# Kernel optimization log

Hardware: AMD Instinct MI355X
Metric: run time of the kernel (lower is better)

## Reference

```python
import jax, jax.numpy as jnp
import numpy as np

N_PROTS = 20000
N_GRAPHS = 16
N = N_PROTS * N_GRAPHS        # 320_000 nodes
F = 128                       # input features
L = 10                        # lat_size (hard-coded in module)
E = 10_240_000                # edges, avg degree 32


def setup_inputs() -> dict:
    key = jax.random.key(0)
    ks = jax.random.split(key, 8)
    x = jax.random.normal(ks[0], (N, F), dtype=jnp.float32)
    edge_index = jax.random.randint(ks[1], (2, E), 0, N, dtype=jnp.int32)
    def lin(k, fan_in, shape):
        return jax.random.uniform(k, shape, jnp.float32, -1.0, 1.0) / np.sqrt(fan_in)
    return {
        "x": x,
        "edge_index": edge_index,
        "W_in": lin(ks[2], F, (F, L)),
        "b_in": jnp.zeros((L,), jnp.float32),
        "W1": lin(ks[3], L, (L, L)),
        "b1": jnp.zeros((L,), jnp.float32),
        "W2": lin(ks[4], L, (L, L)),
        "b2": jnp.zeros((L,), jnp.float32),
        "W_out": lin(ks[5], L, (L, 1)),
        "b_out": jnp.zeros((1,), jnp.float32),
    }


def _gcn_improved(h, row, col, deg_inv_sqrt, W, b):
    # GCNConv(improved=True): A_hat = A + 2I, out = D^-1/2 A_hat D^-1/2 (h W) + b
    hw = h @ W                                   # [N, L]
    norm = deg_inv_sqrt[row] * deg_inv_sqrt[col]  # [E]
    agg = jax.ops.segment_sum(norm[:, None] * hw[row], col, num_segments=N)
    # self-loop with weight 2: contributes 2/deg * hw per node
    agg = agg + (2.0 * deg_inv_sqrt * deg_inv_sqrt)[:, None] * hw
    return agg + b


def reference(x, edge_index, W_in, b_in, W1, b1, W2, b2, W_out, b_out):
    row, col = edge_index[0], edge_index[1]
    # degree incl. self-loop fill value 2.0 (improved)
    deg = jax.ops.segment_sum(jnp.ones((E,), jnp.float32), col, num_segments=N) + 2.0
    deg_inv_sqrt = jax.lax.rsqrt(deg)

    h = jax.nn.relu(x @ W_in + b_in)                         # input_linear + relu
    h = jax.nn.relu(_gcn_improved(h, row, col, deg_inv_sqrt, W1, b1))
    h = jax.nn.relu(_gcn_improved(h, row, col, deg_inv_sqrt, W2, b2))
    out = h @ W_out + b_out                                  # output_linear
    return out.reshape(-1, N_PROTS, 1)
```

## Files before the change

### kernel.cpp

```cpp
#include <hip/hip_runtime.h>

#define NN 320000
#define FF 128
#define EE 10240000
#define NBUK 625
#define CSH 9
#define CLOC 512
#define BCAP2 17280
#define NSLAB 8
#define SLABDIV 40000u
#define KEYS 4096
#define EPB 40000
#define GSTRIDE 16

__global__ __launch_bounds__(1024) void k_bucket(const int* __restrict__ row,
                                                 const int* __restrict__ col,
                                                 int* __restrict__ gcur,
                                                 int* __restrict__ buf) {
  __shared__ int hist[NBUK];
  __shared__ int cur[NBUK];
  int t = threadIdx.x;
  long long e0 = (long long)blockIdx.x * EPB;

  for (int b = t; b < NBUK; b += 1024) hist[b] = 0;
  __syncthreads();

  for (int i = t; i < EPB; i += 1024) {
    atomicAdd(&hist[col[e0 + i] >> CSH], 1);
  }
  __syncthreads();

  for (int b = t; b < NBUK; b += 1024) {
    cur[b] = atomicAdd(&gcur[b], hist[b]);
  }
  __syncthreads();

  for (int i = t; i < EPB; i += 1024) {
    int c = col[e0 + i];
    int r = row[e0 + i];
    int b = c >> CSH;
    int slot = atomicAdd(&cur[b], 1);
    if (slot < BCAP2) buf[(long long)b * BCAP2 + slot] = (r << CSH) | (c & (CLOC - 1));
  }
}

__global__ __launch_bounds__(512) void k_sortdeg(const int* __restrict__ gcur,
                                                 int* __restrict__ buf,
                                                 int* __restrict__ off,
                                                 float* __restrict__ dis) {
  __shared__ int stage[BCAP2];
  __shared__ int hist[KEYS];
  __shared__ int tsum[512];
  int t = threadIdx.x;
  int b = blockIdx.x;
  long long base = (long long)b * BCAP2;
  int cnt = gcur[b]; if (cnt > BCAP2) cnt = BCAP2;

#pragma unroll
  for (int k = 0; k < NSLAB; k++) hist[t * NSLAB + k] = 0;
  __syncthreads();

  for (int i = t; i < cnt; i += 512) {
    int e = buf[base + i];
    stage[i] = e;
    int key = ((e & (CLOC - 1)) << 3) | (int)((unsigned)(e >> CSH) / SLABDIV);
    atomicAdd(&hist[key], 1);
  }
  __syncthreads();

  int mysum = 0;
#pragma unroll
  for (int k = 0; k < NSLAB; k++) mysum += hist[t * NSLAB + k];
  tsum[t] = mysum;
  __syncthreads();
  for (int o = 1; o < 512; o <<= 1) {
    int v = (t >= o) ? tsum[t - o] : 0;
    __syncthreads();
    tsum[t] += v;
    __syncthreads();
  }
  int runbase = tsum[t] - mysum;
  int running = runbase;
#pragma unroll
  for (int k = 0; k < NSLAB; k++) {
    int old = hist[t * NSLAB + k];
    hist[t * NSLAB + k] = running;
    running += old;
  }
  off[b * 513 + t] = runbase;
  if (t == 0) off[b * 513 + 512] = cnt;
  dis[b * CLOC + t] = rsqrtf((float)mysum + 2.0f);
  __syncthreads();

  for (int i = t; i < cnt; i += 512) {
    int e = stage[i];
    int key = ((e & (CLOC - 1)) << 3) | (int)((unsigned)(e >> CSH) / SLABDIV);
    int slot = atomicAdd(&hist[key], 1);
    buf[base + slot] = e >> CSH;
  }
}

__global__ __launch_bounds__(256) void k_h0(const float* __restrict__ x,
                                            const float* __restrict__ Win,
                                            const float* __restrict__ bin,
                                            const float* __restrict__ W1,
                                            const float* __restrict__ dis,
                                            float* __restrict__ g1) {
  int n = blockIdx.x * 256 + threadIdx.x;
  float acc[10];
#pragma unroll
  for (int l = 0; l < 10; l++) acc[l] = bin[l];

  const float4* xr = (const float4*)(x + (long long)n * FF);
#pragma unroll
  for (int j = 0; j < FF / 4; j++) {
    float4 v = xr[j];
    const float* w = Win + (j * 4) * 10;
#pragma unroll
    for (int l = 0; l < 10; l++) acc[l] = fmaf(v.x, w[l], acc[l]);
#pragma unroll
    for (int l = 0; l < 10; l++) acc[l] = fmaf(v.y, w[10 + l], acc[l]);
#pragma unroll
    for (int l = 0; l < 10; l++) acc[l] = fmaf(v.z, w[20 + l], acc[l]);
#pragma unroll
    for (int l = 0; l < 10; l++) acc[l] = fmaf(v.w, w[30 + l], acc[l]);
  }
  float h[10];
#pragma unroll
  for (int l = 0; l < 10; l++) h[l] = fmaxf(acc[l], 0.f);

  float hw[10];
#pragma unroll
  for (int l = 0; l < 10; l++) hw[l] = 0.f;
#pragma unroll
  for (int k = 0; k < 10; k++) {
    const float* wr = W1 + k * 10;
#pragma unroll
    for (int l = 0; l < 10; l++) hw[l] = fmaf(h[k], wr[l], hw[l]);
  }

  float di = dis[n];
  float4* gp = (float4*)(g1 + (long long)n * GSTRIDE);
  gp[0] = make_float4(di * hw[0], di * hw[1], di * hw[2], di * hw[3]);
  gp[1] = make_float4(di * hw[4], di * hw[5], di * hw[6], di * hw[7]);
  gp[2] = make_float4(di * hw[8], di * hw[9], 0.f, 0.f);
}

#define GATHER_RUN(GSRC)                                             \
  {                                                                  \
    int i = s;                                                       \
    for (int k = 0; k < NSLAB; k++) {                                \
      int bound = (k + 1) * (int)SLABDIV;                            \
      while (i < e) {                                                \
        int r = __builtin_nontemporal_load(bb + i);                  \
        if (r >= bound) break;                                       \
        const float4* q = (const float4*)(GSRC + (long long)r * GSTRIDE); \
        float4 A = q[0], B = q[1];                                   \
        float2 C = *(const float2*)(q + 2);                          \
        acc[0] += A.x; acc[1] += A.y; acc[2] += A.z; acc[3] += A.w;  \
        acc[4] += B.x; acc[5] += B.y; acc[6] += B.z; acc[7] += B.w;  \
        acc[8] += C.x; acc[9] += C.y;                                \
        i++;                                                         \
      }                                                              \
      __syncthreads();                                               \
    }                                                                \
  }

__global__ __launch_bounds__(256) void k_scatter_mid(const int* __restrict__ buf,
                                                     const int* __restrict__ off,
                                                     const float* __restrict__ g1,
                                                     const float* __restrict__ dis,
                                                     const float* __restrict__ b1,
                                                     const float* __restrict__ W2,
                                                     float* __restrict__ g2) {
  int n = blockIdx.x * 256 + threadIdx.x;
  int b = n >> CSH;
  int c = n & (CLOC - 1);
  const int* bb = buf + (long long)b * BCAP2;
  int s = off[b * 513 + c];
  int e = off[b * 513 + c + 1];

  float acc[10];
#pragma unroll
  for (int l = 0; l < 10; l++) acc[l] = 0.f;
  GATHER_RUN(g1);

  float di = dis[n];
  float tw = 2.0f * di;
  const float4* g1p = (const float4*)(g1 + (long long)n * GSTRIDE);
  float4 ga = g1p[0], gb = g1p[1];
  float2 gc = *(const float2*)(g1p + 2);

  float h[10];
  h[0] = fmaxf(fmaf(di, acc[0], fmaf(tw, ga.x, b1[0])), 0.f);
  h[1] = fmaxf(fmaf(di, acc[1], fmaf(tw, ga.y, b1[1])), 0.f);
  h[2] = fmaxf(fmaf(di, acc[2], fmaf(tw, ga.z, b1[2])), 0.f);
  h[3] = fmaxf(fmaf(di, acc[3], fmaf(tw, ga.w, b1[3])), 0.f);
  h[4] = fmaxf(fmaf(di, acc[4], fmaf(tw, gb.x, b1[4])), 0.f);
  h[5] = fmaxf(fmaf(di, acc[5], fmaf(tw, gb.y, b1[5])), 0.f);
  h[6] = fmaxf(fmaf(di, acc[6], fmaf(tw, gb.z, b1[6])), 0.f);
  h[7] = fmaxf(fmaf(di, acc[7], fmaf(tw, gb.w, b1[7])), 0.f);
  h[8] = fmaxf(fmaf(di, acc[8], fmaf(tw, gc.x, b1[8])), 0.f);
  h[9] = fmaxf(fmaf(di, acc[9], fmaf(tw, gc.y, b1[9])), 0.f);

  float hw[10];
#pragma unroll
  for (int l = 0; l < 10; l++) hw[l] = 0.f;
#pragma unroll
  for (int k = 0; k < 10; k++) {
    const float* wr = W2 + k * 10;
#pragma unroll
    for (int l = 0; l < 10; l++) hw[l] = fmaf(h[k], wr[l], hw[l]);
  }

  float4* gp = (float4*)(g2 + (long long)n * GSTRIDE);
  gp[0] = make_float4(di * hw[0], di * hw[1], di * hw[2], di * hw[3]);
  gp[1] = make_float4(di * hw[4], di * hw[5], di * hw[6], di * hw[7]);
  gp[2] = make_float4(di * hw[8], di * hw[9], 0.f, 0.f);
}

__global__ __launch_bounds__(256) void k_scatter_out(const int* __restrict__ buf,
                                                     const int* __restrict__ off,
                                                     const float* __restrict__ g2,
                                                     const float* __restrict__ dis,
                                                     const float* __restrict__ b2,
                                                     const float* __restrict__ Wout,
                                                     const float* __restrict__ bout,
                                                     float* __restrict__ out) {
  int n = blockIdx.x * 256 + threadIdx.x;
  int b = n >> CSH;
  int c = n & (CLOC - 1);
  const int* bb = buf + (long long)b * BCAP2;
  int s = off[b * 513 + c];
  int e = off[b * 513 + c + 1];

  float acc[10];
#pragma unroll
  for (int l = 0; l < 10; l++) acc[l] = 0.f;
  GATHER_RUN(g2);

  float di = dis[n];
  float tw = 2.0f * di;
  const float4* g2p = (const float4*)(g2 + (long long)n * GSTRIDE);
  float4 ga = g2p[0], gb = g2p[1];
  float2 gc = *(const float2*)(g2p + 2);

  float h[10];
  h[0] = fmaxf(fmaf(di, acc[0], fmaf(tw, ga.x, b2[0])), 0.f);
  h[1] = fmaxf(fmaf(di, acc[1], fmaf(tw, ga.y, b2[1])), 0.f);
  h[2] = fmaxf(fmaf(di, acc[2], fmaf(tw, ga.z, b2[2])), 0.f);
  h[3] = fmaxf(fmaf(di, acc[3], fmaf(tw, ga.w, b2[3])), 0.f);
  h[4] = fmaxf(fmaf(di, acc[4], fmaf(tw, gb.x, b2[4])), 0.f);
  h[5] = fmaxf(fmaf(di, acc[5], fmaf(tw, gb.y, b2[5])), 0.f);
  h[6] = fmaxf(fmaf(di, acc[6], fmaf(tw, gb.z, b2[6])), 0.f);
  h[7] = fmaxf(fmaf(di, acc[7], fmaf(tw, gb.w, b2[7])), 0.f);
  h[8] = fmaxf(fmaf(di, acc[8], fmaf(tw, gc.x, b2[8])), 0.f);
  h[9] = fmaxf(fmaf(di, acc[9], fmaf(tw, gc.y, b2[9])), 0.f);

  float o = bout[0];
#pragma unroll
  for (int l = 0; l < 10; l++) o = fmaf(h[l], Wout[l], o);
  out[n] = o;
}

extern "C" void kernel_launch(void* const* d_in, const int* in_sizes, int n_in,
                              void* d_out, int out_size, void* d_ws, size_t ws_size,
                              hipStream_t stream) {
  const float* x    = (const float*)d_in[0];
  const int*   ei   = (const int*)d_in[1];
  const float* Win  = (const float*)d_in[2];
  const float* bin  = (const float*)d_in[3];
  const float* W1   = (const float*)d_in[4];
  const float* b1   = (const float*)d_in[5];
  const float* W2   = (const float*)d_in[6];
  const float* b2   = (const float*)d_in[7];
  const float* Wout = (const float*)d_in[8];
  const float* bout = (const float*)d_in[9];
  float* out = (float*)d_out;

  int*   buf  = (int*)d_ws;
  int*   gcur = buf + (long long)NBUK * BCAP2;
  int*   off  = gcur + 1024;
  float* dis  = (float*)(off + 321024);
  float* g1   = dis + NN;
  float* g2   = g1 + GSTRIDE * NN;

  const int* row = ei;
  const int* col = ei + EE;

  hipMemsetAsync(gcur, 0, NBUK * sizeof(int), stream);
  k_bucket<<<256, 1024, 0, stream>>>(row, col, gcur, buf);
  k_sortdeg<<<NBUK, 512, 0, stream>>>(gcur, buf, off, dis);
  k_h0<<<NN / 256, 256, 0, stream>>>(x, Win, bin, W1, dis, g1);
  k_scatter_mid<<<NN / 256, 256, 0, stream>>>(buf, off, g1, dis, b1, W2, g2);
  k_scatter_out<<<NN / 256, 256, 0, stream>>>(buf, off, g2, dis, b2, Wout, bout, out);
}
```

Measured before the change: 1.074 ms.

## Add grid-wide slab barriers to gather kernels for L2 locality

Launches one 512-thread block per bucket and makes all blocks move through the source-row slabs together, using a bounded global atomic counter barrier before each slab. The aim is that every block reads the same slab of g at the same time, so the working set stays resident in cache and random gathers hit it more often. The cost is eight grid-wide barriers with spin-waiting. The spin is capped, so if the 625 blocks cannot all be resident at once the barrier degrades into a timeout instead of a deadlock.

New measurement: 1.759 ms. +63.8%, slower.

```diff
diff --git a/kernel.cpp b/kernel.cpp
--- a/kernel.cpp
+++ b/kernel.cpp
@@ -146,10 +146,25 @@
   gp[2] = make_float4(di * hw[8], di * hw[9], 0.f, 0.f);
 }
 
-#define GATHER_RUN(GSRC)                                             \
+__device__ __forceinline__ void slab_sync(int* cnt, int target) {
+  __syncthreads();
+  if (threadIdx.x == 0) {
+    __hip_atomic_fetch_add(cnt, 1, __ATOMIC_RELAXED, __HIP_MEMORY_SCOPE_AGENT);
+    int spins = 0;
+    while (__hip_atomic_load(cnt, __ATOMIC_RELAXED, __HIP_MEMORY_SCOPE_AGENT) < target &&
+           spins < 8192) {
+      ++spins;
+      __builtin_amdgcn_s_sleep(2);
+    }
+  }
+  __syncthreads();
+}
+
+#define GATHER_RUN(GSRC, SYNC)                                       \
   {                                                                  \
     int i = s;                                                       \
     for (int k = 0; k < NSLAB; k++) {                                \
+      slab_sync(&(SYNC)[k], NBUK);                                   \
       int bound = (k + 1) * (int)SLABDIV;                            \
       while (i < e) {                                                \
         int r = __builtin_nontemporal_load(bb + i);                  \
@@ -162,28 +177,28 @@
         acc[8] += C.x; acc[9] += C.y;                                \
         i++;                                                         \
       }                                                              \
-      __syncthreads();                                               \
     }                                                                \
   }
 
-__global__ __launch_bounds__(256) void k_scatter_mid(const int* __restrict__ buf,
+__global__ __launch_bounds__(512) void k_scatter_mid(const int* __restrict__ buf,
                                                      const int* __restrict__ off,
                                                      const float* __restrict__ g1,
                                                      const float* __restrict__ dis,
                                                      const float* __restrict__ b1,
                                                      const float* __restrict__ W2,
+                                                     int* __restrict__ gsync,
                                                      float* __restrict__ g2) {
-  int n = blockIdx.x * 256 + threadIdx.x;
-  int b = n >> CSH;
-  int c = n & (CLOC - 1);
+  int b = blockIdx.x;
+  int t = threadIdx.x;
+  int n = b * CLOC + t;
   const int* bb = buf + (long long)b * BCAP2;
-  int s = off[b * 513 + c];
-  int e = off[b * 513 + c + 1];
+  int s = off[b * 513 + t];
+  int e = off[b * 513 + t + 1];
 
   float acc[10];
 #pragma unroll
   for (int l = 0; l < 10; l++) acc[l] = 0.f;
-  GATHER_RUN(g1);
+  GATHER_RUN(g1, gsync);
 
   float di = dis[n];
   float tw = 2.0f * di;
@@ -219,25 +234,26 @@
   gp[2] = make_float4(di * hw[8], di * hw[9], 0.f, 0.f);
 }
 
-__global__ __launch_bounds__(256) void k_scatter_out(const int* __restrict__ buf,
+__global__ __launch_bounds__(512) void k_scatter_out(const int* __restrict__ buf,
                                                      const int* __restrict__ off,
                                                      const float* __restrict__ g2,
                                                      const float* __restrict__ dis,
                                                      const float* __restrict__ b2,
                                                      const float* __restrict__ Wout,
                                                      const float* __restrict__ bout,
+                                                     int* __restrict__ gsync,
                                                      float* __restrict__ out) {
-  int n = blockIdx.x * 256 + threadIdx.x;
-  int b = n >> CSH;
-  int c = n & (CLOC - 1);
+  int b = blockIdx.x;
+  int t = threadIdx.x;
+  int n = b * CLOC + t;
   const int* bb = buf + (long long)b * BCAP2;
-  int s = off[b * 513 + c];
-  int e = off[b * 513 + c + 1];
+  int s = off[b * 513 + t];
+  int e = off[b * 513 + t + 1];
 
   float acc[10];
 #pragma unroll
   for (int l = 0; l < 10; l++) acc[l] = 0.f;
-  GATHER_RUN(g2);
+  GATHER_RUN(g2, gsync);
 
   float di = dis[n];
   float tw = 2.0f * di;
@@ -278,20 +294,22 @@
   const float* bout = (const float*)d_in[9];
   float* out = (float*)d_out;
 
-  int*   buf  = (int*)d_ws;
-  int*   gcur = buf + (long long)NBUK * BCAP2;
-  int*   off  = gcur + 1024;
-  float* dis  = (float*)(off + 321024);
-  float* g1   = dis + NN;
-  float* g2   = g1 + GSTRIDE * NN;
+  int*   buf    = (int*)d_ws;
+  int*   gcur   = buf + (long long)NBUK * BCAP2;
+  int*   gsyncA = gcur + 640;
+  int*   gsyncB = gcur + 656;
+  int*   off    = gcur + 1024;
+  float* dis    = (float*)(off + 321024);
+  float* g1     = dis + NN;
+  float* g2     = g1 + GSTRIDE * NN;
 
   const int* row = ei;
   const int* col = ei + EE;
 
-  hipMemsetAsync(gcur, 0, NBUK * sizeof(int), stream);
+  hipMemsetAsync(gcur, 0, 1024 * sizeof(int), stream);
   k_bucket<<<256, 1024, 0, stream>>>(row, col, gcur, buf);
   k_sortdeg<<<NBUK, 512, 0, stream>>>(gcur, buf, off, dis);
   k_h0<<<NN / 256, 256, 0, stream>>>(x, Win, bin, W1, dis, g1);
-  k_scatter_mid<<<NN / 256, 256, 0, stream>>>(buf, off, g1, dis, b1, W2, g2);
-  k_scatter_out<<<NN / 256, 256, 0, stream>>>(buf, off, g2, dis, b2, Wout, bout, out);
-}
+  k_scatter_mid<<<NBUK, 512, 0, stream>>>(buf, off, g1, dis, b1, W2, gsyncA, g2);
+  k_scatter_out<<<NBUK, 512, 0, stream>>>(buf, off, g2, dis, b2, Wout, bout, gsyncB, out);
+}
```
